# Performance work log

Measured on AMD Instinct MI355X. Metric: run time of the kernel, lower is better.

The kernel has to match this reference:

```python
import jax, jax.numpy as jnp
import numpy as np

N = 4096      # total nodes (target + context)
T = 1024      # target nodes
C = N - T     # context nodes
F = 128       # raw node feature dim
H = 512       # num_hids
HEADS = 16    # num_heads
D = H // HEADS
WIN = 2       # window_size
L = 2         # num_layers
E_T = 65536   # edges: target queries -> context keys
E_C = 98304   # edges: context queries -> target keys
EDGE_ENC = 8
EDGE_DIST = 8
SCALE = D ** -0.5


def setup_inputs():
    key = jax.random.key(0)
    ks = iter(jax.random.split(key, 40))
    s = 0.02
    rn = lambda shp, sc=1.0: jax.random.normal(next(ks), shp, jnp.float32) * sc
    return {
        "node_feats": rn((N, F)),
        "edge_emb_table": rn((EDGE_ENC * WIN, H), s),
        "edge_dist_emb_table": rn((EDGE_DIST, H), s),
        "w_node": rn((F, H), s), "b_node": jnp.zeros((H,), jnp.float32),
        "w_edge_enc": rn((H, HEADS), s), "b_edge_enc": jnp.zeros((HEADS,), jnp.float32),
        "w_edge_dist": rn((H, HEADS), s), "b_edge_dist": jnp.zeros((HEADS,), jnp.float32),
        "ln1_g": jnp.ones((L, H), jnp.float32), "ln1_b": jnp.zeros((L, H), jnp.float32),
        "attn1_w": rn((L, 4, H, H), s), "attn1_b": jnp.zeros((L, 4, H), jnp.float32),
        "attn2_w": rn((L, 4, H, H), s), "attn2_b": jnp.zeros((L, 4, H), jnp.float32),
        "ln2_g": jnp.ones((L, H), jnp.float32), "ln2_b": jnp.zeros((L, H), jnp.float32),
        "ffn_w1": rn((L, H, H), s), "ffn_b1": jnp.zeros((L, H), jnp.float32),
        "ffn_w2": rn((L, H, H), s), "ffn_b2": jnp.zeros((L, H), jnp.float32),
        "edge_encodes": jax.random.randint(next(ks), (N, N, WIN), 0, EDGE_ENC * WIN, jnp.int32),
        "edge_dist_encodes": jax.random.randint(next(ks), (N, N), 0, EDGE_DIST, jnp.int32),
        "target_sparse_row": jax.random.randint(next(ks), (E_T,), 0, T, jnp.int32),
        "target_sparse_col": jax.random.randint(next(ks), (E_T,), 0, C, jnp.int32),
        "context_sparse_row": jax.random.randint(next(ks), (E_C,), 0, C, jnp.int32),
        "context_sparse_col": jax.random.randint(next(ks), (E_C,), 0, T, jnp.int32),
        "target_node_size": T,
    }


def _ln(x, g, b, eps=1e-5):
    m = jnp.mean(x, -1, keepdims=True)
    v = jnp.mean((x - m) ** 2, -1, keepdims=True)
    return (x - m) * jax.lax.rsqrt(v + eps) * g + b


def _seg_softmax(x, idx, n):
    # scatter-max / scatter-sum softmax over edges grouped by row index
    m = jax.ops.segment_max(x, idx, num_segments=n)
    m = jnp.where(jnp.isfinite(m), m, 0.0)  # empty segments
    e = jnp.exp(x - m[idx])
    s = jax.ops.segment_sum(e, idx, num_segments=n)
    return e / (s[idx] + 1e-16)


def _emb(table, idx):
    # nn.Embedding(max_norm=True): looked-up rows renormed to L2 norm <= 1
    e = table[idx]
    nrm = jnp.linalg.norm(e, axis=-1, keepdims=True)
    return e / jnp.maximum(nrm, 1.0)


def _mha(yq, ykv, w, b, bias, row, col, n_out):
    # w: [4,H,H] = q,k,v,o projections; b: [4,H]
    q = (yq @ w[0] + b[0]).reshape(-1, HEADS, D)
    k = (ykv @ w[1] + b[1]).reshape(-1, HEADS, D)
    v = (ykv @ w[2] + b[2]).reshape(-1, HEADS, D)
    s = jnp.einsum('ehd,ehd->eh', q[row], k[col]) * SCALE + bias  # [E,HEADS]
    a = _seg_softmax(s, row, n_out)
    o = jax.ops.segment_sum(a[:, :, None] * v[col], row, num_segments=n_out)
    return o.reshape(-1, H) @ w[3] + b[3]


def _forward(node_feats, edge_emb_table, edge_dist_emb_table, w_node, b_node,
             w_edge_enc, b_edge_enc, w_edge_dist, b_edge_dist,
             ln1_g, ln1_b, attn1_w, attn1_b, attn2_w, attn2_b,
             ln2_g, ln2_b, ffn_w1, ffn_b1, ffn_w2, ffn_b2,
             edge_encodes, edge_dist_encodes,
             target_sparse_row, target_sparse_col,
             context_sparse_row, context_sparse_col, Tn):
    Cn = node_feats.shape[0] - Tn

    def bias_for(rows, cols):
        # get_encodings: mean over window of edge embedding, plus dist embedding
        e1 = jnp.mean(_emb(edge_emb_table, edge_encodes[rows, cols]), axis=-2)  # [E,H]
        b1 = e1 @ w_edge_enc + b_edge_enc
        e2 = _emb(edge_dist_emb_table, edge_dist_encodes[rows, cols])           # [E,H]
        b2 = e2 @ w_edge_dist + b_edge_dist
        return b1 + b2                                                           # [E,HEADS]

    attn_bias_target = bias_for(target_sparse_row, target_sparse_col + Tn)
    attn_bias_context = bias_for(context_sparse_row + Tn, context_sparse_col)

    x = node_feats @ w_node + b_node
    for l in range(L):
        y = _ln(x, ln1_g[l], ln1_b[l])
        y_t, y_c = y[:Tn], y[Tn:]
        out1 = _mha(y_t, y_c, attn1_w[l], attn1_b[l], attn_bias_target,
                    target_sparse_row, target_sparse_col, Tn)    # [T,H]
        out2 = _mha(y_c, y_t, attn2_w[l], attn2_b[l], attn_bias_context,
                    context_sparse_row, context_sparse_col, Cn)  # [C,H]
        # original code: y_all = cat([y_target_, y_context_]) = [attn2 out, attn1 out]
        x = x + jnp.concatenate([out2, out1], axis=0)
        y = _ln(x, ln2_g[l], ln2_b[l])
        y = jax.nn.gelu(y @ ffn_w1[l] + ffn_b1[l], approximate=False) @ ffn_w2[l] + ffn_b2[l]
        x = x + y
    return x


def reference(node_feats, edge_emb_table, edge_dist_emb_table, w_node, b_node,
              w_edge_enc, b_edge_enc, w_edge_dist, b_edge_dist,
              ln1_g, ln1_b, attn1_w, attn1_b, attn2_w, attn2_b,
              ln2_g, ln2_b, ffn_w1, ffn_b1, ffn_w2, ffn_b2,
              edge_encodes, edge_dist_encodes,
              target_sparse_row, target_sparse_col,
              context_sparse_row, context_sparse_col, target_node_size):
    return _forward(node_feats, edge_emb_table, edge_dist_emb_table, w_node, b_node,
                    w_edge_enc, b_edge_enc, w_edge_dist, b_edge_dist,
                    ln1_g, ln1_b, attn1_w, attn1_b, attn2_w, attn2_b,
                    ln2_g, ln2_b, ffn_w1, ffn_b1, ffn_w2, ffn_b2,
                    edge_encodes, edge_dist_encodes,
                    target_sparse_row, target_sparse_col,
                    context_sparse_row, context_sparse_col, target_node_size)
```

## Files before the change

### kernel.cpp

```cpp
#include <hip/hip_runtime.h>
#include <math.h>

#define N_NODES 4096
#define T_NODES 1024
#define C_NODES 3072
#define F_IN    128
#define H_DIM   512
#define HEADS   16
#define D_HEAD  32
#define E_T     65536
#define E_C     98304
#define SCALE_QK 0.17677669529663687f

typedef __attribute__((ext_vector_type(8))) short short8;
typedef __attribute__((ext_vector_type(4))) float f32x4;

struct ushort4_t { unsigned short x, y, z, w; };

__device__ inline unsigned short f2bf(float f) {
    unsigned u = __float_as_uint(f);
    unsigned r = (u + 0x7fffu + ((u >> 16) & 1u)) >> 16;
    return (unsigned short)r;
}
__device__ inline float bf2f(unsigned short u) {
    return __uint_as_float(((unsigned)u) << 16);
}

__device__ inline void gload16(const void* g, void* l) {
    __builtin_amdgcn_global_load_lds(
        (const __attribute__((address_space(1))) unsigned int*)g,
        (__attribute__((address_space(3))) unsigned int*)l, 16, 0, 0);
}

struct TD { const float* src[20]; unsigned short* dst[20]; };

__global__ void prep_kernel(TD d, const float* __restrict__ w_node, unsigned short* __restrict__ wnT,
                            const float* __restrict__ nf, unsigned short* __restrict__ nfb)
{
    int z = blockIdx.z;
    __shared__ float tile[32][33];
    int tr = threadIdx.x >> 5, tc = threadIdx.x & 31;
    if (z < 20) {
        const float* src = d.src[z];
        unsigned short* dst = d.dst[z];
        int r0 = blockIdx.y * 32, c0 = blockIdx.x * 32;
        #pragma unroll
        for (int p = 0; p < 4; ++p) tile[tr + 8*p][tc] = src[(size_t)(r0 + tr + 8*p)*512 + c0 + tc];
        __syncthreads();
        #pragma unroll
        for (int p = 0; p < 4; ++p) dst[(size_t)(c0 + tr + 8*p)*512 + r0 + tc] = f2bf(tile[tc][tr + 8*p]);
    } else if (z == 20) {
        if (blockIdx.y >= 4) return;
        int r0 = blockIdx.y * 32, c0 = blockIdx.x * 32;
        #pragma unroll
        for (int p = 0; p < 4; ++p) tile[tr + 8*p][tc] = w_node[(size_t)(r0 + tr + 8*p)*512 + c0 + tc];
        __syncthreads();
        #pragma unroll
        for (int p = 0; p < 4; ++p) wnT[(size_t)(c0 + tr + 8*p)*128 + r0 + tc] = f2bf(tile[tc][tr + 8*p]);
    } else {
        int gid = (blockIdx.y * 16 + blockIdx.x) * 256 + threadIdx.x;
        #pragma unroll
        for (int rep = 0; rep < 2; ++rep) {
            int i = gid + rep * 65536;
            float4 v = ((const float4*)nf)[i];
            ushort4_t o = { f2bf(v.x), f2bf(v.y), f2bf(v.z), f2bf(v.w) };
            ((ushort4_t*)nfb)[i] = o;
        }
    }
}

__global__ void proj_kernel(const float* __restrict__ emb, const float* __restrict__ dist_emb,
                            const float* __restrict__ w_enc, const float* __restrict__ w_dist,
                            const float* __restrict__ a1b, const float* __restrict__ a2b,
                            float* __restrict__ P1, float* __restrict__ P2,
                            float* __restrict__ bct, float* __restrict__ bcc)
{
    if (blockIdx.x == 96) {
        int t = threadIdx.x;
        for (int l = 0; l < 2; ++l)
            for (int i = t; i < 512; i += 256) {
                bct[l*1536 + i]        = a1b[(l*4+0)*512 + i];
                bct[l*1536 + 512 + i]  = a2b[(l*4+1)*512 + i];
                bct[l*1536 + 1024 + i] = a2b[(l*4+2)*512 + i];
                bcc[l*1536 + i]        = a1b[(l*4+1)*512 + i];
                bcc[l*1536 + 512 + i]  = a1b[(l*4+2)*512 + i];
                bcc[l*1536 + 1024 + i] = a2b[(l*4+0)*512 + i];
            }
        return;
    }
    int wid = threadIdx.x >> 6, lane = threadIdx.x & 63;
    int o = blockIdx.x * 4 + wid;
    const float* src; const float* wm; float* dst; int h;
    if (o < 256) { src = emb      + (size_t)(o >> 4) * 512; wm = w_enc;  h = o & 15;  dst = P1 + o; }
    else { int o2 = o - 256; src = dist_emb + (size_t)(o2 >> 4) * 512; wm = w_dist; h = o2 & 15; dst = P2 + o2; }
    float4 v0 = ((const float4*)src)[lane*2];
    float4 v1 = ((const float4*)src)[lane*2+1];
    float nrm = v0.x*v0.x + v0.y*v0.y + v0.z*v0.z + v0.w*v0.w
              + v1.x*v1.x + v1.y*v1.y + v1.z*v1.z + v1.w*v1.w;
    int f0 = lane * 8;
    float dt = v0.x*wm[(f0+0)*16+h] + v0.y*wm[(f0+1)*16+h] + v0.z*wm[(f0+2)*16+h] + v0.w*wm[(f0+3)*16+h]
             + v1.x*wm[(f0+4)*16+h] + v1.y*wm[(f0+5)*16+h] + v1.z*wm[(f0+6)*16+h] + v1.w*wm[(f0+7)*16+h];
    #pragma unroll
    for (int s = 1; s < 64; s <<= 1) { nrm += __shfl_xor(nrm, s, 64); dt += __shfl_xor(dt, s, 64); }
    if (lane == 0) *dst = dt / fmaxf(sqrtf(nrm), 1.0f);
}

__global__ void hist2_kernel(const int* __restrict__ t_row, const int* __restrict__ c_row,
                             int* __restrict__ cnt_t, int* __restrict__ cnt_c) {
    int i = blockIdx.x * 256 + threadIdx.x;
    if (i < E_T) atomicAdd(&cnt_t[t_row[i]], 1);
    else atomicAdd(&cnt_c[c_row[i - E_T]], 1);
}

__global__ void scan2_kernel(const int* __restrict__ cnt_t, int* __restrict__ off_t, int* __restrict__ cur_t,
                             const int* __restrict__ cnt_c, int* __restrict__ off_c, int* __restrict__ cur_c) {
    const int* counts; int* offsets; int* cursor; int n;
    if (blockIdx.x == 0) { counts = cnt_t; offsets = off_t; cursor = cur_t; n = T_NODES; }
    else                 { counts = cnt_c; offsets = off_c; cursor = cur_c; n = C_NODES; }
    __shared__ int lds[1024];
    int t = threadIdx.x;
    int c = (n + 1023) / 1024;
    int base = t * c;
    int s = 0;
    for (int j = 0; j < c; ++j) { int i = base + j; if (i < n) s += counts[i]; }
    lds[t] = s;
    __syncthreads();
    for (int d = 1; d < 1024; d <<= 1) {
        int v = (t >= d) ? lds[t-d] : 0;
        __syncthreads();
        lds[t] += v;
        __syncthreads();
    }
    int run = lds[t] - s;
    for (int j = 0; j < c; ++j) {
        int i = base + j;
        if (i < n) { offsets[i] = run; cursor[i] = run; run += counts[i]; }
    }
    if (t == 1023) offsets[n] = lds[1023];
}

__global__ void scatter2_kernel(const int* __restrict__ t_row, const int* __restrict__ c_row,
                                int* __restrict__ cur_t, int* __restrict__ cur_c,
                                int* __restrict__ perm_t, int* __restrict__ perm_c) {
    int i = blockIdx.x * 256 + threadIdx.x;
    if (i < E_T) { int p = atomicAdd(&cur_t[t_row[i]], 1); perm_t[p] = i; }
    else { int j = i - E_T; int p = atomicAdd(&cur_c[c_row[j]], 1); perm_c[p] = j; }
}

__global__ void bias2_kernel(const int* __restrict__ t_row, const int* __restrict__ t_col,
                             const int* __restrict__ c_row, const int* __restrict__ c_col,
                             const int* __restrict__ perm_t, const int* __restrict__ perm_c,
                             const int* __restrict__ enc, const int* __restrict__ dist,
                             const float* __restrict__ P1, const float* __restrict__ P2,
                             const float* __restrict__ b_enc, const float* __restrict__ b_dist,
                             float* __restrict__ biasp_t, float* __restrict__ biasp_c,
                             int* __restrict__ colp_t, int* __restrict__ colp_c)
{
    __shared__ float sP1[256], sP2[128], sb[16];
    int t = threadIdx.x;
    sP1[t] = P1[t];
    if (t < 128) sP2[t] = P2[t];
    if (t < 16)  sb[t]  = b_enc[t] + b_dist[t];
    __syncthreads();
    int gi = blockIdx.x * 256 + t;
    if (gi < E_T) {
        int i = gi; int e = perm_t[i];
        long r = t_row[e]; long c = t_col[e];
        long idx = r * N_NODES + c + T_NODES;
        int i1 = enc[idx*2], i2 = enc[idx*2+1], j = dist[idx];
        colp_t[i] = (int)c;
        #pragma unroll
        for (int h = 0; h < 16; ++h)
            biasp_t[(size_t)h*E_T + i] = 0.5f*(sP1[i1*16+h] + sP1[i2*16+h]) + sP2[j*16+h] + sb[h];
    } else {
        int i = gi - E_T; int e = perm_c[i];
        long r = c_row[e] + T_NODES; long c = c_col[e];
        long idx = r * N_NODES + c;
        int i1 = enc[idx*2], i2 = enc[idx*2+1], j = dist[idx];
        colp_c[i] = (int)c;
        #pragma unroll
        for (int h = 0; h < 16; ++h)
            biasp_c[(size_t)h*E_C + i] = 0.5f*(sP1[i1*16+h] + sP1[i2*16+h]) + sP2[j*16+h] + sb[h];
    }
}

__global__ void ln_kernel(const float* __restrict__ x, const float* __restrict__ g,
                          const float* __restrict__ b, unsigned short* __restrict__ y, int M) {
    int wave = threadIdx.x >> 6;
    int lane = threadIdx.x & 63;
    int row = blockIdx.x * 4 + wave;
    if (row >= M) return;
    const float4* xr = (const float4*)(x + (size_t)row * H_DIM);
    float4 a = xr[lane*2], c4 = xr[lane*2+1];
    float s  = a.x + a.y + a.z + a.w + c4.x + c4.y + c4.z + c4.w;
    float sq = a.x*a.x + a.y*a.y + a.z*a.z + a.w*a.w + c4.x*c4.x + c4.y*c4.y + c4.z*c4.z + c4.w*c4.w;
    #pragma unroll
    for (int o = 1; o < 64; o <<= 1) { s += __shfl_xor(s, o, 64); sq += __shfl_xor(sq, o, 64); }
    float mean = s * (1.0f/512.0f);
    float var  = sq * (1.0f/512.0f) - mean*mean;
    float inv  = rsqrtf(var + 1e-5f);
    const float4* gp = (const float4*)g;
    const float4* bp = (const float4*)b;
    float4 g0 = gp[lane*2], g1 = gp[lane*2+1];
    float4 b0 = bp[lane*2], b1 = bp[lane*2+1];
    ushort4_t o0 = { f2bf((a.x-mean)*inv*g0.x + b0.x), f2bf((a.y-mean)*inv*g0.y + b0.y),
                     f2bf((a.z-mean)*inv*g0.z + b0.z), f2bf((a.w-mean)*inv*g0.w + b0.w) };
    ushort4_t o1 = { f2bf((c4.x-mean)*inv*g1.x + b1.x), f2bf((c4.y-mean)*inv*g1.y + b1.y),
                     f2bf((c4.z-mean)*inv*g1.z + b1.z), f2bf((c4.w-mean)*inv*g1.w + b1.w) };
    ushort4_t* yr = (ushort4_t*)(y + (size_t)row * H_DIM);
    yr[lane*2] = o0; yr[lane*2+1] = o1;
}

template <int MODE>
__global__ __launch_bounds__(256) void gemm_bf16(
    const unsigned short* __restrict__ A, int lda,
    const unsigned short* __restrict__ Wa, const unsigned short* __restrict__ Wb, int ldb,
    const float* __restrict__ biasa, const float* __restrict__ biasb,
    void* __restrict__ Cout, int ldc, int K, int mswitch)
{
    __shared__ unsigned short As[2][128*32];
    __shared__ unsigned short Bs[2][64*32];
    int tid  = threadIdx.x;
    int wid  = tid >> 6, lane = tid & 63;
    int wm   = wid >> 1, wn = wid & 1;
    int m0   = blockIdx.y * 128, n0 = blockIdx.x * 64;
    const unsigned short* BT = (m0 >= mswitch) ? Wb : Wa;
    const float* bias        = (m0 >= mswitch) ? biasb : biasa;

    int srow  = lane >> 2;
    int sslot = lane & 3;
    const unsigned short* Ag0 = A  + (size_t)(m0 + wid*32 + srow)*lda + sslot*8;
    const unsigned short* Ag1 = Ag0 + (size_t)16*lda;
    const unsigned short* Bg0 = BT + (size_t)(n0 + wid*16 + srow)*ldb + sslot*8;

    f32x4 acc[4][2] = {};
    int NT = K >> 5;

    auto stage = [&](int bsel, int kt) {
        char* abase = (char*)&As[bsel][0] + wid*2048;
        char* bbase = (char*)&Bs[bsel][0] + wid*1024;
        gload16(Ag0 + kt*32, abase);
        gload16(Ag1 + kt*32, abase + 1024);
        gload16(Bg0 + kt*32, bbase);
    };

    stage(0, 0);
    __syncthreads();
    int cur = 0;
    int arowf = wm*64 + (lane & 15);
    int kslot = (lane >> 4) * 8;
    for (int kt = 0; kt < NT; ++kt) {
        if (kt + 1 < NT) stage(cur ^ 1, kt + 1);
        const unsigned short* as = &As[cur][0];
        const unsigned short* bs = &Bs[cur][0];
        short8 af[4], bf[2];
        #pragma unroll
        for (int fm = 0; fm < 4; ++fm)
            af[fm] = *(const short8*)&as[(arowf + fm*16)*32 + kslot];
        #pragma unroll
        for (int fn = 0; fn < 2; ++fn)
            bf[fn] = *(const short8*)&bs[(wn*32 + fn*16 + (lane & 15))*32 + kslot];
        #pragma unroll
        for (int fm = 0; fm < 4; ++fm)
            #pragma unroll
            for (int fn = 0; fn < 2; ++fn)
                acc[fm][fn] = __builtin_amdgcn_mfma_f32_16x16x32_bf16(af[fm], bf[fn], acc[fm][fn], 0, 0, 0);
        __syncthreads();
        cur ^= 1;
    }

    int crow = m0 + wm*64 + (lane >> 4)*4;
    int ccol = n0 + wn*32 + (lane & 15);
    #pragma unroll
    for (int fn = 0; fn < 2; ++fn) {
        float bv = bias[ccol + fn*16];
        #pragma unroll
        for (int fm = 0; fm < 4; ++fm) {
            #pragma unroll
            for (int j = 0; j < 4; ++j) {
                float val = acc[fm][fn][j] + bv;
                size_t off = (size_t)(crow + fm*16 + j)*ldc + ccol + fn*16;
                if (MODE == 0) {
                    ((float*)Cout)[off] = val;
                } else if (MODE == 1) {
                    float gl = 0.5f * val * (1.0f + erff(val * 0.70710678118654752f));
                    ((unsigned short*)Cout)[off] = f2bf(gl);
                } else if (MODE == 2) {
                    ((float*)Cout)[off] += val;
                } else {
                    ((unsigned short*)Cout)[off] = f2bf(val);
                }
            }
        }
    }
}

__global__ __launch_bounds__(256) void attn_fused(
    const unsigned short* __restrict__ qkv,
    const float* __restrict__ biasp_t, const float* __restrict__ biasp_c,
    const int* __restrict__ off_t, const int* __restrict__ colp_t,
    const int* __restrict__ off_c, const int* __restrict__ colp_c,
    unsigned short* __restrict__ ob)
{
    __shared__ float2 lds_pc[8][2][32];
    int grp = threadIdx.x >> 5, lane = threadIdx.x & 31;
    int g = blockIdx.x * 8 + grp;

    int r, h, orow;
    size_t qoff, kbase, vbase;
    const float* bias_h; const int* offs; const int* colp;
    if (g < T_NODES * HEADS) {
        r = g >> 4; h = g & 15;
        qoff  = (size_t)r * 1536 + h*32;
        kbase = (size_t)T_NODES * 1536 + h*32;
        vbase = (size_t)T_NODES * 1536 + 512 + h*32;
        bias_h = biasp_t + (size_t)h * E_T;
        offs = off_t; colp = colp_t;
        orow = C_NODES + r;
    } else {
        int g2 = g - T_NODES * HEADS;
        r = g2 >> 4; h = g2 & 15;
        qoff  = (size_t)(T_NODES + r) * 1536 + 1024 + h*32;
        kbase = 512 + h*32;
        vbase = 1024 + h*32;
        bias_h = biasp_c + (size_t)h * E_C;
        offs = off_c; colp = colp_c;
        orow = r;
    }

    float qf[32];
    {
        const short8* qp = (const short8*)(qkv + qoff);
        #pragma unroll
        for (int jj = 0; jj < 4; ++jj) {
            short8 qq = qp[jj];
            #pragma unroll
            for (int j2 = 0; j2 < 8; ++j2) qf[jj*8+j2] = bf2f((unsigned short)qq[j2]);
        }
    }

    int beg = offs[r], end = offs[r+1];
    float lsum = 0.f;
    float acc0 = 0.f, acc1 = 0.f, acc2 = 0.f, acc3 = 0.f;
    const unsigned short* vb = qkv + vbase;

    #pragma unroll 2
    for (int i0 = beg; i0 < end; i0 += 32) {
        int par = ((i0 - beg) >> 5) & 1;
        float2* pc = &lds_pc[grp][par][0];
        const float4* pcr4 = (const float4*)pc;

        int i = i0 + lane;
        bool ok = i < end;
        int c = ok ? colp[i] : 0;
        float pw = 0.f;
        {
            float bv = ok ? bias_h[i] : 0.f;
            const short8* kp = (const short8*)(qkv + kbase + (size_t)c * 1536);
            short8 k0 = kp[0], k1 = kp[1], k2 = kp[2], k3 = kp[3];
            float d0 = 0.f, d1 = 0.f;
            #pragma unroll
            for (int j2 = 0; j2 < 8; ++j2) {
                d0 += qf[j2]    * bf2f((unsigned short)k0[j2]);
                d1 += qf[8+j2]  * bf2f((unsigned short)k1[j2]);
                d0 += qf[16+j2] * bf2f((unsigned short)k2[j2]);
                d1 += qf[24+j2] * bf2f((unsigned short)k3[j2]);
            }
            float s = (d0 + d1) * SCALE_QK + bv;
            if (ok) pw = __expf(s);
        }
        lsum += pw;
        pc[lane] = float2{ pw, __int_as_float(c) };

        #pragma unroll
        for (int j = 0; j < 8; ++j) {
            float4 p01 = pcr4[j*2];
            float4 p23 = pcr4[j*2 + 1];
            int c0 = __float_as_int(p01.y), c1 = __float_as_int(p01.w);
            int c2 = __float_as_int(p23.y), c3 = __float_as_int(p23.w);
            acc0 += p01.x * bf2f(vb[(size_t)c0*1536 + lane]);
            acc1 += p01.z * bf2f(vb[(size_t)c1*1536 + lane]);
            acc2 += p23.x * bf2f(vb[(size_t)c2*1536 + lane]);
            acc3 += p23.z * bf2f(vb[(size_t)c3*1536 + lane]);
        }
    }

    #pragma unroll
    for (int o2 = 16; o2 >= 1; o2 >>= 1) lsum += __shfl_xor(lsum, o2, 32);
    float acc = (acc0 + acc1) + (acc2 + acc3);
    ob[(size_t)orow * H_DIM + h*32 + lane] = f2bf(acc / (lsum + 1e-16f));
}

extern "C" void kernel_launch(void* const* d_in, const int* in_sizes, int n_in,
                              void* d_out, int out_size, void* d_ws, size_t ws_size,
                              hipStream_t stream)
{
    const float* node_feats = (const float*)d_in[0];
    const float* edge_emb   = (const float*)d_in[1];
    const float* dist_emb   = (const float*)d_in[2];
    const float* w_node     = (const float*)d_in[3];
    const float* b_node     = (const float*)d_in[4];
    const float* w_enc      = (const float*)d_in[5];
    const float* b_enc      = (const float*)d_in[6];
    const float* w_dist     = (const float*)d_in[7];
    const float* b_dist     = (const float*)d_in[8];
    const float* ln1_g      = (const float*)d_in[9];
    const float* ln1_b      = (const float*)d_in[10];
    const float* attn1_w    = (const float*)d_in[11];
    const float* attn1_b    = (const float*)d_in[12];
    const float* attn2_w    = (const float*)d_in[13];
    const float* attn2_b    = (const float*)d_in[14];
    const float* ln2_g      = (const float*)d_in[15];
    const float* ln2_b      = (const float*)d_in[16];
    const float* ffn_w1     = (const float*)d_in[17];
    const float* ffn_b1     = (const float*)d_in[18];
    const float* ffn_w2     = (const float*)d_in[19];
    const float* ffn_b2     = (const float*)d_in[20];
    const int* enc          = (const int*)d_in[21];
    const int* dist         = (const int*)d_in[22];
    const int* t_row        = (const int*)d_in[23];
    const int* t_col        = (const int*)d_in[24];
    const int* c_row        = (const int*)d_in[25];
    const int* c_col        = (const int*)d_in[26];

    float* x = (float*)d_out;

    char* w = (char*)d_ws;
    auto alloc = [&](size_t bytes) { char* p = w; w += (bytes + 255) & ~(size_t)255; return p; };

    unsigned short* qkv  = (unsigned short*)alloc((size_t)N_NODES*1536*2);
    unsigned short* nfb  = qkv;
    unsigned short* h1   = qkv;
    unsigned short* yb   = (unsigned short*)alloc((size_t)N_NODES*H_DIM*2);
    unsigned short* ob   = (unsigned short*)alloc((size_t)N_NODES*H_DIM*2);
    float* biasp_t       = (float*)alloc((size_t)HEADS*E_T*4);
    float* biasp_c       = (float*)alloc((size_t)HEADS*E_C*4);
    int* colp_t          = (int*)alloc((size_t)E_T*4);
    int* colp_c          = (int*)alloc((size_t)E_C*4);
    int* cnt_t           = (int*)alloc(T_NODES*4);
    int* cnt_c           = (int*)alloc(C_NODES*4);
    int* off_t           = (int*)alloc((T_NODES+1)*4);
    int* cur_t           = (int*)alloc(T_NODES*4);
    int* perm_t          = (int*)alloc((size_t)E_T*4);
    int* off_c           = (int*)alloc((C_NODES+1)*4);
    int* cur_c           = (int*)alloc(C_NODES*4);
    int* perm_c          = (int*)alloc((size_t)E_C*4);
    float* P1            = (float*)alloc(256*4);
    float* P2            = (float*)alloc(128*4);
    unsigned short* wcat_t = (unsigned short*)alloc((size_t)2*1536*512*2);
    unsigned short* wcat_c = (unsigned short*)alloc((size_t)2*1536*512*2);
    unsigned short* wo1    = (unsigned short*)alloc((size_t)2*512*512*2);
    unsigned short* wo2    = (unsigned short*)alloc((size_t)2*512*512*2);
    unsigned short* wf1    = (unsigned short*)alloc((size_t)2*512*512*2);
    unsigned short* wf2    = (unsigned short*)alloc((size_t)2*512*512*2);
    unsigned short* wnT    = (unsigned short*)alloc((size_t)H_DIM*F_IN*2);
    float* bcat_t        = (float*)alloc(2*1536*4);
    float* bcat_c        = (float*)alloc(2*1536*4);

    const size_t SZ = 512*512;
    const int BIG = 1 << 30;

    TD td;
    for (int l = 0; l < 2; ++l) {
        int b = l*10;
        td.src[b+0] = attn1_w + (size_t)(l*4+0)*SZ;  td.dst[b+0] = wcat_t + (size_t)l*1536*512;
        td.src[b+1] = attn2_w + (size_t)(l*4+1)*SZ;  td.dst[b+1] = wcat_t + (size_t)l*1536*512 + SZ;
        td.src[b+2] = attn2_w + (size_t)(l*4+2)*SZ;  td.dst[b+2] = wcat_t + (size_t)l*1536*512 + 2*SZ;
        td.src[b+3] = attn1_w + (size_t)(l*4+1)*SZ;  td.dst[b+3] = wcat_c + (size_t)l*1536*512;
        td.src[b+4] = attn1_w + (size_t)(l*4+2)*SZ;  td.dst[b+4] = wcat_c + (size_t)l*1536*512 + SZ;
        td.src[b+5] = attn2_w + (size_t)(l*4+0)*SZ;  td.dst[b+5] = wcat_c + (size_t)l*1536*512 + 2*SZ;
        td.src[b+6] = attn1_w + (size_t)(l*4+3)*SZ;  td.dst[b+6] = wo1 + (size_t)l*SZ;
        td.src[b+7] = attn2_w + (size_t)(l*4+3)*SZ;  td.dst[b+7] = wo2 + (size_t)l*SZ;
        td.src[b+8] = ffn_w1  + (size_t)l*SZ;        td.dst[b+8] = wf1 + (size_t)l*SZ;
        td.src[b+9] = ffn_w2  + (size_t)l*SZ;        td.dst[b+9] = wf2 + (size_t)l*SZ;
    }
    prep_kernel<<<dim3(16,16,22), 256, 0, stream>>>(td, w_node, wnT, node_feats, nfb);
    proj_kernel<<<97, 256, 0, stream>>>(edge_emb, dist_emb, w_enc, w_dist,
                                        attn1_b, attn2_b, P1, P2, bcat_t, bcat_c);

    hipMemsetAsync(cnt_t, 0, (T_NODES + C_NODES)*4, stream);
    hist2_kernel<<<(E_T+E_C)/256, 256, 0, stream>>>(t_row, c_row, cnt_t, cnt_c);
    scan2_kernel<<<2, 1024, 0, stream>>>(cnt_t, off_t, cur_t, cnt_c, off_c, cur_c);
    scatter2_kernel<<<(E_T+E_C)/256, 256, 0, stream>>>(t_row, c_row, cur_t, cur_c, perm_t, perm_c);
    bias2_kernel<<<(E_T+E_C)/256, 256, 0, stream>>>(t_row, t_col, c_row, c_col, perm_t, perm_c,
                                                    enc, dist, P1, P2, b_enc, b_dist,
                                                    biasp_t, biasp_c, colp_t, colp_c);

    gemm_bf16<0><<<dim3(8, 32), 256, 0, stream>>>(nfb, F_IN, wnT, wnT, F_IN,
                                                  b_node, b_node, x, H_DIM, F_IN, BIG);

    for (int l = 0; l < 2; ++l) {
        ln_kernel<<<N_NODES/4, 256, 0, stream>>>(x, ln1_g + l*H_DIM, ln1_b + l*H_DIM, yb, N_NODES);

        gemm_bf16<3><<<dim3(24, 32), 256, 0, stream>>>(yb, H_DIM,
            wcat_t + (size_t)l*1536*512, wcat_c + (size_t)l*1536*512, H_DIM,
            bcat_t + l*1536, bcat_c + l*1536, qkv, 1536, H_DIM, T_NODES);

        attn_fused<<<(T_NODES + C_NODES)*HEADS/8, 256, 0, stream>>>(
            qkv, biasp_t, biasp_c, off_t, colp_t, off_c, colp_c, ob);

        gemm_bf16<2><<<dim3(8, 32), 256, 0, stream>>>(ob, H_DIM,
            wo2 + (size_t)l*SZ, wo1 + (size_t)l*SZ, H_DIM,
            attn2_b + (size_t)(l*4+3)*H_DIM, attn1_b + (size_t)(l*4+3)*H_DIM,
            x, H_DIM, H_DIM, C_NODES);

        ln_kernel<<<N_NODES/4, 256, 0, stream>>>(x, ln2_g + l*H_DIM, ln2_b + l*H_DIM, yb, N_NODES);
        gemm_bf16<1><<<dim3(8, 32), 256, 0, stream>>>(yb, H_DIM,
            wf1 + (size_t)l*SZ, wf1 + (size_t)l*SZ, H_DIM,
            ffn_b1 + l*H_DIM, ffn_b1 + l*H_DIM, h1, H_DIM, H_DIM, BIG);
        gemm_bf16<2><<<dim3(8, 32), 256, 0, stream>>>(h1, H_DIM,
            wf2 + (size_t)l*SZ, wf2 + (size_t)l*SZ, H_DIM,
            ffn_b2 + l*H_DIM, ffn_b2 + l*H_DIM, x, H_DIM, H_DIM, BIG);
    }
}
```

Before: 315.8 us.

## Restructure sparse attention to per-edge-lane V accumulation with LDS transpose reduction

Each lane now owns one edge and loads that edge's full 32-wide V row as vectors, accumulating a 32-element per-lane partial output, instead of broadcasting probabilities and column indices through LDS and gathering V one scalar per lane. At the end, partial outputs are transposed through padded shared memory and summed across lanes. The next chunk's column index and bias are also prefetched one iteration ahead. The aim is to replace many scattered 2-byte V gathers with coalesced 64-byte vector loads per edge, at the cost of 32 extra accumulator registers per thread and an LDS reduction at the end.

```diff
diff --git a/kernel.cpp b/kernel.cpp
--- a/kernel.cpp
+++ b/kernel.cpp
@@ -302,7 +302,7 @@
     const int* __restrict__ off_c, const int* __restrict__ colp_c,
     unsigned short* __restrict__ ob)
 {
-    __shared__ float2 lds_pc[8][2][32];
+    __shared__ float trans[8][32*36];
     int grp = threadIdx.x >> 5, lane = threadIdx.x & 31;
     int g = blockIdx.x * 8 + grp;
 
@@ -341,54 +341,67 @@
 
     int beg = offs[r], end = offs[r+1];
     float lsum = 0.f;
-    float acc0 = 0.f, acc1 = 0.f, acc2 = 0.f, acc3 = 0.f;
-    const unsigned short* vb = qkv + vbase;
-
-    #pragma unroll 2
+    float accd[32];
+    #pragma unroll
+    for (int d = 0; d < 32; ++d) accd[d] = 0.f;
+
+    bool ok = (beg + lane) < end;
+    int   c_cur  = ok ? colp[beg + lane]   : 0;
+    float bv_cur = ok ? bias_h[beg + lane] : 0.f;
+
     for (int i0 = beg; i0 < end; i0 += 32) {
-        int par = ((i0 - beg) >> 5) & 1;
-        float2* pc = &lds_pc[grp][par][0];
-        const float4* pcr4 = (const float4*)pc;
-
-        int i = i0 + lane;
-        bool ok = i < end;
-        int c = ok ? colp[i] : 0;
-        float pw = 0.f;
-        {
-            float bv = ok ? bias_h[i] : 0.f;
-            const short8* kp = (const short8*)(qkv + kbase + (size_t)c * 1536);
-            short8 k0 = kp[0], k1 = kp[1], k2 = kp[2], k3 = kp[3];
-            float d0 = 0.f, d1 = 0.f;
-            #pragma unroll
-            for (int j2 = 0; j2 < 8; ++j2) {
-                d0 += qf[j2]    * bf2f((unsigned short)k0[j2]);
-                d1 += qf[8+j2]  * bf2f((unsigned short)k1[j2]);
-                d0 += qf[16+j2] * bf2f((unsigned short)k2[j2]);
-                d1 += qf[24+j2] * bf2f((unsigned short)k3[j2]);
-            }
-            float s = (d0 + d1) * SCALE_QK + bv;
-            if (ok) pw = __expf(s);
+        int   c  = c_cur;
+        float bv = bv_cur;
+        bool  okc = (i0 + lane) < end;
+        int in = i0 + 32 + lane;
+        bool okn = in < end;
+        c_cur  = okn ? colp[in]   : 0;
+        bv_cur = okn ? bias_h[in] : 0.f;
+
+        const short8* kp = (const short8*)(qkv + kbase + (size_t)c * 1536);
+        const short8* vp = (const short8*)(qkv + vbase + (size_t)c * 1536);
+        short8 k0 = kp[0], k1 = kp[1], k2 = kp[2], k3 = kp[3];
+        short8 v0 = vp[0], v1 = vp[1], v2 = vp[2], v3 = vp[3];
+
+        float d0 = 0.f, d1 = 0.f;
+        #pragma unroll
+        for (int j2 = 0; j2 < 8; ++j2) {
+            d0 += qf[j2]    * bf2f((unsigned short)k0[j2]);
+            d1 += qf[8+j2]  * bf2f((unsigned short)k1[j2]);
+            d0 += qf[16+j2] * bf2f((unsigned short)k2[j2]);
+            d1 += qf[24+j2] * bf2f((unsigned short)k3[j2]);
         }
+        float s = (d0 + d1) * SCALE_QK + bv;
+        float pw = okc ? __expf(s) : 0.f;
         lsum += pw;
-        pc[lane] = float2{ pw, __int_as_float(c) };
-
-        #pragma unroll
-        for (int j = 0; j < 8; ++j) {
-            float4 p01 = pcr4[j*2];
-            float4 p23 = pcr4[j*2 + 1];
-            int c0 = __float_as_int(p01.y), c1 = __float_as_int(p01.w);
-            int c2 = __float_as_int(p23.y), c3 = __float_as_int(p23.w);
-            acc0 += p01.x * bf2f(vb[(size_t)c0*1536 + lane]);
-            acc1 += p01.z * bf2f(vb[(size_t)c1*1536 + lane]);
-            acc2 += p23.x * bf2f(vb[(size_t)c2*1536 + lane]);
-            acc3 += p23.z * bf2f(vb[(size_t)c3*1536 + lane]);
+
+        #pragma unroll
+        for (int j2 = 0; j2 < 8; ++j2) {
+            accd[j2]    += pw * bf2f((unsigned short)v0[j2]);
+            accd[8+j2]  += pw * bf2f((unsigned short)v1[j2]);
+            accd[16+j2] += pw * bf2f((unsigned short)v2[j2]);
+            accd[24+j2] += pw * bf2f((unsigned short)v3[j2]);
         }
     }
 
     #pragma unroll
     for (int o2 = 16; o2 >= 1; o2 >>= 1) lsum += __shfl_xor(lsum, o2, 32);
-    float acc = (acc0 + acc1) + (acc2 + acc3);
-    ob[(size_t)orow * H_DIM + h*32 + lane] = f2bf(acc / (lsum + 1e-16f));
+
+    float* tr = &trans[grp][0];
+    #pragma unroll
+    for (int j = 0; j < 8; ++j)
+        *(float4*)&tr[lane*36 + j*4] = float4{ accd[j*4], accd[j*4+1], accd[j*4+2], accd[j*4+3] };
+
+    float o0 = 0.f, o1 = 0.f, o2s = 0.f, o3 = 0.f;
+    #pragma unroll
+    for (int e = 0; e < 32; e += 4) {
+        o0  += tr[(e+0)*36 + lane];
+        o1  += tr[(e+1)*36 + lane];
+        o2s += tr[(e+2)*36 + lane];
+        o3  += tr[(e+3)*36 + lane];
+    }
+    float osum = (o0 + o1) + (o2s + o3);
+    ob[(size_t)orow * H_DIM + h*32 + lane] = f2bf(osum / (lsum + 1e-16f));
 }
 
 extern "C" void kernel_launch(void* const* d_in, const int* in_sizes, int n_in,
```

After: 315.1 us. No clear change (-0.2%).

## Process all heads per wave in sparse attention with edge-major bias layout

Applied to the files above, without the earlier changes.

Attention now assigns one 64-lane wave per query row covering all 16 heads. Each lane holds 8 dims, and the 32-dim dot product per head is reduced with two shuffles. Gathering K/V is now a single contiguous 1 KB row read per edge instead of 16 separate per-head gathers, and the LDS staging of probabilities is gone. The bias buffer is transposed to edge-major so each edge's 16 head biases sit together. In exchange there is less parallelism (4096 waves instead of 65536 32-lane groups), and the serial per-edge loop over degree-length lists could expose latency.

```diff
diff --git a/kernel.cpp b/kernel.cpp
--- a/kernel.cpp
+++ b/kernel.cpp
@@ -171,7 +171,7 @@
         colp_t[i] = (int)c;
         #pragma unroll
         for (int h = 0; h < 16; ++h)
-            biasp_t[(size_t)h*E_T + i] = 0.5f*(sP1[i1*16+h] + sP1[i2*16+h]) + sP2[j*16+h] + sb[h];
+            biasp_t[(size_t)i*16 + h] = 0.5f*(sP1[i1*16+h] + sP1[i2*16+h]) + sP2[j*16+h] + sb[h];
     } else {
         int i = gi - E_T; int e = perm_c[i];
         long r = c_row[e] + T_NODES; long c = c_col[e];
@@ -180,7 +180,7 @@
         colp_c[i] = (int)c;
         #pragma unroll
         for (int h = 0; h < 16; ++h)
-            biasp_c[(size_t)h*E_C + i] = 0.5f*(sP1[i1*16+h] + sP1[i2*16+h]) + sP2[j*16+h] + sb[h];
+            biasp_c[(size_t)i*16 + h] = 0.5f*(sP1[i1*16+h] + sP1[i2*16+h]) + sP2[j*16+h] + sb[h];
     }
 }
 
@@ -302,93 +302,73 @@
     const int* __restrict__ off_c, const int* __restrict__ colp_c,
     unsigned short* __restrict__ ob)
 {
-    __shared__ float2 lds_pc[8][2][32];
-    int grp = threadIdx.x >> 5, lane = threadIdx.x & 31;
-    int g = blockIdx.x * 8 + grp;
-
-    int r, h, orow;
-    size_t qoff, kbase, vbase;
-    const float* bias_h; const int* offs; const int* colp;
-    if (g < T_NODES * HEADS) {
-        r = g >> 4; h = g & 15;
-        qoff  = (size_t)r * 1536 + h*32;
-        kbase = (size_t)T_NODES * 1536 + h*32;
-        vbase = (size_t)T_NODES * 1536 + 512 + h*32;
-        bias_h = biasp_t + (size_t)h * E_T;
-        offs = off_t; colp = colp_t;
+    int wave = threadIdx.x >> 6, lane = threadIdx.x & 63;
+    int g = blockIdx.x * 4 + wave;
+
+    int r, orow, rowbase, kcol;
+    size_t qoff;
+    const float* biasE; const int* offs; const int* colp;
+    if (g < T_NODES) {
+        r = g;
+        qoff = (size_t)r * 1536;
+        rowbase = T_NODES; kcol = 0;
+        biasE = biasp_t; offs = off_t; colp = colp_t;
         orow = C_NODES + r;
     } else {
-        int g2 = g - T_NODES * HEADS;
-        r = g2 >> 4; h = g2 & 15;
-        qoff  = (size_t)(T_NODES + r) * 1536 + 1024 + h*32;
-        kbase = 512 + h*32;
-        vbase = 1024 + h*32;
-        bias_h = biasp_c + (size_t)h * E_C;
-        offs = off_c; colp = colp_c;
+        r = g - T_NODES;
+        qoff = (size_t)(T_NODES + r) * 1536 + 1024;
+        rowbase = 0; kcol = 512;
+        biasE = biasp_c; offs = off_c; colp = colp_c;
         orow = r;
     }
 
-    float qf[32];
+    float qf[8];
     {
-        const short8* qp = (const short8*)(qkv + qoff);
-        #pragma unroll
-        for (int jj = 0; jj < 4; ++jj) {
-            short8 qq = qp[jj];
-            #pragma unroll
-            for (int j2 = 0; j2 < 8; ++j2) qf[jj*8+j2] = bf2f((unsigned short)qq[j2]);
-        }
-    }
+        short8 qq = *(const short8*)(qkv + qoff + lane*8);
+        #pragma unroll
+        for (int j = 0; j < 8; ++j) qf[j] = bf2f((unsigned short)qq[j]);
+    }
+    int h4 = lane >> 2;
 
     int beg = offs[r], end = offs[r+1];
     float lsum = 0.f;
-    float acc0 = 0.f, acc1 = 0.f, acc2 = 0.f, acc3 = 0.f;
-    const unsigned short* vb = qkv + vbase;
-
-    #pragma unroll 2
-    for (int i0 = beg; i0 < end; i0 += 32) {
-        int par = ((i0 - beg) >> 5) & 1;
-        float2* pc = &lds_pc[grp][par][0];
-        const float4* pcr4 = (const float4*)pc;
-
-        int i = i0 + lane;
-        bool ok = i < end;
-        int c = ok ? colp[i] : 0;
-        float pw = 0.f;
-        {
-            float bv = ok ? bias_h[i] : 0.f;
-            const short8* kp = (const short8*)(qkv + kbase + (size_t)c * 1536);
-            short8 k0 = kp[0], k1 = kp[1], k2 = kp[2], k3 = kp[3];
-            float d0 = 0.f, d1 = 0.f;
+    float acc[8];
+    #pragma unroll
+    for (int j = 0; j < 8; ++j) acc[j] = 0.f;
+
+    for (int i0 = beg; i0 < end; i0 += 4) {
+        bool okk[4]; int cc[4]; float bb[4];
+        short8 kk[4], vv[4];
+        #pragma unroll
+        for (int u = 0; u < 4; ++u) {
+            int ii = i0 + u;
+            okk[u] = ii < end;
+            cc[u]  = okk[u] ? colp[ii] : 0;
+            bb[u]  = okk[u] ? biasE[(size_t)ii*16 + h4] : 0.f;
+            const unsigned short* base = qkv + (size_t)(rowbase + cc[u])*1536 + kcol + lane*8;
+            kk[u] = *(const short8*)base;
+            vv[u] = *(const short8*)(base + 512);
+        }
+        #pragma unroll
+        for (int u = 0; u < 4; ++u) {
+            float d = 0.f;
             #pragma unroll
-            for (int j2 = 0; j2 < 8; ++j2) {
-                d0 += qf[j2]    * bf2f((unsigned short)k0[j2]);
-                d1 += qf[8+j2]  * bf2f((unsigned short)k1[j2]);
-                d0 += qf[16+j2] * bf2f((unsigned short)k2[j2]);
-                d1 += qf[24+j2] * bf2f((unsigned short)k3[j2]);
-            }
-            float s = (d0 + d1) * SCALE_QK + bv;
-            if (ok) pw = __expf(s);
+            for (int j = 0; j < 8; ++j) d += qf[j] * bf2f((unsigned short)kk[u][j]);
+            d += __shfl_xor(d, 1, 64);
+            d += __shfl_xor(d, 2, 64);
+            float s = d * SCALE_QK + bb[u];
+            float pw = okk[u] ? __expf(s) : 0.f;
+            lsum += pw;
+            #pragma unroll
+            for (int j = 0; j < 8; ++j) acc[j] += pw * bf2f((unsigned short)vv[u][j]);
         }
-        lsum += pw;
-        pc[lane] = float2{ pw, __int_as_float(c) };
-
-        #pragma unroll
-        for (int j = 0; j < 8; ++j) {
-            float4 p01 = pcr4[j*2];
-            float4 p23 = pcr4[j*2 + 1];
-            int c0 = __float_as_int(p01.y), c1 = __float_as_int(p01.w);
-            int c2 = __float_as_int(p23.y), c3 = __float_as_int(p23.w);
-            acc0 += p01.x * bf2f(vb[(size_t)c0*1536 + lane]);
-            acc1 += p01.z * bf2f(vb[(size_t)c1*1536 + lane]);
-            acc2 += p23.x * bf2f(vb[(size_t)c2*1536 + lane]);
-            acc3 += p23.z * bf2f(vb[(size_t)c3*1536 + lane]);
-        }
-    }
-
-    #pragma unroll
-    for (int o2 = 16; o2 >= 1; o2 >>= 1) lsum += __shfl_xor(lsum, o2, 32);
-    float acc = (acc0 + acc1) + (acc2 + acc3);
-    ob[(size_t)orow * H_DIM + h*32 + lane] = f2bf(acc / (lsum + 1e-16f));
+    }
+
+    float inv = 1.0f / (lsum + 1e-16f);
+    ushort4_t o0 = { f2bf(acc[0]*inv), f2bf(acc[1]*inv), f2bf(acc[2]*inv), f2bf(acc[3]*inv) };
+    ushort4_t o1 = { f2bf(acc[4]*inv), f2bf(acc[5]*inv), f2bf(acc[6]*inv), f2bf(acc[7]*inv) };
+    ushort4_t* op = (ushort4_t*)(ob + (size_t)orow * H_DIM + lane*8);
+    op[0] = o0; op[1] = o1;
 }
 
 extern "C" void kernel_launch(void* const* d_in, const int* in_sizes, int n_in,
@@ -433,8 +413,8 @@
     unsigned short* h1   = qkv;
     unsigned short* yb   = (unsigned short*)alloc((size_t)N_NODES*H_DIM*2);
     unsigned short* ob   = (unsigned short*)alloc((size_t)N_NODES*H_DIM*2);
-    float* biasp_t       = (float*)alloc((size_t)HEADS*E_T*4);
-    float* biasp_c       = (float*)alloc((size_t)HEADS*E_C*4);
+    float* biasp_t       = (float*)alloc((size_t)E_T*HEADS*4);
+    float* biasp_c       = (float*)alloc((size_t)E_C*HEADS*4);
     int* colp_t          = (int*)alloc((size_t)E_T*4);
     int* colp_c          = (int*)alloc((size_t)E_C*4);
     int* cnt_t           = (int*)alloc(T_NODES*4);
@@ -496,7 +476,7 @@
             wcat_t + (size_t)l*1536*512, wcat_c + (size_t)l*1536*512, H_DIM,
             bcat_t + l*1536, bcat_c + l*1536, qkv, 1536, H_DIM, T_NODES);
 
-        attn_fused<<<(T_NODES + C_NODES)*HEADS/8, 256, 0, stream>>>(
+        attn_fused<<<N_NODES/4, 256, 0, stream>>>(
             qkv, biasp_t, biasp_c, off_t, colp_t, off_c, colp_c, ob);
 
         gemm_bf16<2><<<dim3(8, 32), 256, 0, stream>>>(ob, H_DIM,
```

Result: faster. 295.7 us (-6.4%).
